# Optimization experiments

Hardware: AMD Instinct MI355X
Metric: run time of the kernel (lower is better)

Reference implementation:

```python
import jax, jax.numpy as jnp
import numpy as np

PAD = 1
STRIDE = (1, 1)
TEMPERATURE = 1.0


def setup_inputs() -> dict:
    key = jax.random.key(0)
    ks = jax.random.split(key, 5)
    x = jax.random.normal(ks[0], (16, 256, 56, 56), dtype=jnp.float32)
    kernels = jax.random.normal(ks[1], (8, 256, 256, 3, 3), dtype=jnp.float32)
    w1 = jax.random.normal(ks[2], (256, 64), dtype=jnp.float32) * 0.0625
    b1 = jnp.zeros((64,), dtype=jnp.float32)
    w2 = jax.random.normal(ks[3], (64, 8), dtype=jnp.float32) * 0.125
    b2 = jnp.zeros((8,), dtype=jnp.float32)
    return {"x": x, "kernels": kernels, "w1": w1, "b1": b1, "w2": w2, "b2": b2}


def _forward(x, kernels, w1, b1, w2, b2):
    # Attention: global average pool -> MLP -> softmax over kernels
    pooled = jnp.mean(x, axis=(2, 3))                      # [B, C]
    h = jax.nn.relu(pooled @ w1 + b1)                      # [B, H]
    scores = h @ w2 + b2                                   # [B, K]
    alphas = jax.nn.softmax(scores / TEMPERATURE, axis=-1) # [B, K]

    # Per-sample mixed kernels: [B, O, I, kh, kw]
    weighted = jnp.einsum('bk,koihw->boihw', alphas, kernels)

    # Per-sample conv2d (groups=1), vectorized over batch
    def conv_one(xi, wi):
        return jax.lax.conv_general_dilated(
            xi[None], wi, STRIDE, [(PAD, PAD), (PAD, PAD)],
            dimension_numbers=('NCHW', 'OIHW', 'NCHW'))[0]

    return jax.vmap(conv_one)(x, weighted)                 # [B, O, H, W]


def reference(x, kernels, w1, b1, w2, b2):
    return _forward(x, kernels, w1, b1, w2, b2)
```

## Files before the change

kernel.cpp:

```cpp
#include <hip/hip_runtime.h>
#include <hip/hip_bf16.h>
#include <stdint.h>

typedef __attribute__((ext_vector_type(8))) short bf16x8;
typedef __attribute__((ext_vector_type(4))) float f32x4;

#define BATCH 16
#define CH    256
#define HW    56
#define HWHW  3136
#define NK    8

#define XPT_BYTES   30408704ul
#define WK_BYTES    18874368ul
#define POOL_BYTES  16384ul
#define ALPHA_BYTES 512ul

__device__ __forceinline__ void gl_lds16(const void* g, void* l) {
    __builtin_amdgcn_global_load_lds((const __attribute__((address_space(1))) uint32_t*)g,
                                     (__attribute__((address_space(3))) uint32_t*)l, 16, 0, 0);
}

__device__ __forceinline__ float bf16bits_to_f32(short h) {
    return __uint_as_float(((uint32_t)(uint16_t)h) << 16);
}

__global__ void __launch_bounds__(256, 2)
xpose_pool_kernel(const float* __restrict__ x, __hip_bfloat16* __restrict__ xp,
                  float* __restrict__ pooled) {
    __shared__ short tile[2 * 56 * 256];
    const int tid = threadIdx.x;
    const int ys  = blockIdx.x;
    const int b   = blockIdx.y;
    const int y0  = ys * 2;

    const float* xb = x + (size_t)b * CH * HWHW + (size_t)y0 * HW;
    for (int it = 0; it < 28; ++it) {
        int idx = it * 256 + tid;
        int ch  = idx / 28;
        int xi  = idx - ch * 28;
        int r   = xi / 14;
        int x4  = (xi - r * 14) * 4;
        const float4 v = *(const float4*)(xb + (size_t)ch * HWHW + r * HW + x4);
        const float* vf = (const float*)&v;
#pragma unroll
        for (int j = 0; j < 4; ++j) {
            __hip_bfloat16 h = __float2bfloat16(vf[j]);
            tile[(r * 56 + x4 + j) * 256 + (ch ^ (((x4 & 7) | j) << 3))] = *(const short*)&h;
        }
    }
    __syncthreads();

    {
        float s = 0.f;
        const int ch = tid;
        for (int r = 0; r < 2; ++r)
            for (int xx = 0; xx < 56; ++xx)
                s += bf16bits_to_f32(tile[(r * 56 + xx) * 256 + (ch ^ ((xx & 7) << 3))]);
        atomicAdd(&pooled[b * 256 + ch], s * (1.0f / 3136.0f));
    }

    __hip_bfloat16* dst0 = xp + ((size_t)(b * 58 + y0 + 1) * 64 + 1) * 256;
    for (int it = 0; it < 14; ++it) {
        int idx = it * 256 + tid;
        int ch0 = (idx & 31) * 8;
        int pos = idx >> 5;
        int r = pos / 56, xx = pos - (pos / 56) * 56;
        bf16x8 vv = *(const bf16x8*)&tile[(r * 56 + xx) * 256 + (ch0 ^ ((xx & 7) << 3))];
        *(bf16x8*)(dst0 + ((size_t)(r * 64 + xx)) * 256 + ch0) = vv;
    }

    bf16x8 z = {};
    if (tid < 128) {
        int r   = tid >> 6;
        int c2  = (tid >> 5) & 1;
        int ch0 = (tid & 31) * 8;
        *(bf16x8*)(xp + ((size_t)(b * 58 + y0 + 1 + r) * 64 + (c2 ? 57 : 0)) * 256 + ch0) = z;
    }
    if (ys == 0 || ys == 27) {
        int p = (ys == 0) ? 0 : 57;
        __hip_bfloat16* rowp = xp + (size_t)(b * 58 + p) * 64 * 256;
        for (int it = tid; it < 2048; it += 256)
            *(bf16x8*)(rowp + (size_t)it * 8) = z;
    }
}

__global__ void mlp_kernel(const float* __restrict__ pooled,
                           const float* __restrict__ w1, const float* __restrict__ b1,
                           const float* __restrict__ w2, const float* __restrict__ b2,
                           float* __restrict__ alphas) {
    __shared__ float hs[16][64];
    __shared__ float sc[16][8];
    int t = threadIdx.x;
    for (int idx = t; idx < 16 * 64; idx += 256) {
        int b = idx >> 6, j = idx & 63;
        float acc = b1[j];
        const float* pb = pooled + b * 256;
        for (int c = 0; c < 256; ++c) acc += pb[c] * w1[c * 64 + j];
        hs[b][j] = fmaxf(acc, 0.0f);
    }
    __syncthreads();
    if (t < 128) {
        int b = t >> 3, k = t & 7;
        float acc = b2[k];
        for (int j = 0; j < 64; ++j) acc += hs[b][j] * w2[j * 8 + k];
        sc[b][k] = acc;
    }
    __syncthreads();
    if (t < 16) {
        float m = -1e30f;
        for (int k = 0; k < 8; ++k) m = fmaxf(m, sc[t][k]);
        float s = 0.f, e[8];
        for (int k = 0; k < 8; ++k) { e[k] = expf(sc[t][k] - m); s += e[k]; }
        float inv = 1.0f / s;
        for (int k = 0; k < 8; ++k) alphas[t * 8 + k] = e[k] * inv;
    }
}

__global__ void wmix_kernel(const float* __restrict__ kern, const float* __restrict__ alphas,
                            __hip_bfloat16* __restrict__ wk) {
    __shared__ float al[16][8];
    int t = threadIdx.x;
    if (t < 128) al[t >> 3][t & 7] = alphas[t];
    __syncthreads();
    int idx = blockIdx.x * 256 + t;
    float kv[8][9];
    const float* kp = kern + (size_t)idx * 9;
#pragma unroll
    for (int k = 0; k < 8; ++k)
#pragma unroll
        for (int q = 0; q < 9; ++q) kv[k][q] = kp[(size_t)k * 589824 + q];
#pragma unroll 1
    for (int b = 0; b < 16; ++b) {
#pragma unroll
        for (int q = 0; q < 9; ++q) {
            float acc = 0.f;
#pragma unroll
            for (int k = 0; k < 8; ++k) acc += al[b][k] * kv[k][q];
            wk[(((size_t)(b * 9 + q) * 256) << 8) + idx] = __float2bfloat16(acc);
        }
    }
}

__global__ void __launch_bounds__(256, 2)
conv_kernel(const __hip_bfloat16* __restrict__ xpT, const __hip_bfloat16* __restrict__ wk,
            float* __restrict__ out) {
    __shared__ short lds_x[2][6 * 64 * 32];
    __shared__ short lds_a[2][128 * 32];

    const int tid   = threadIdx.x;
    const int lane  = tid & 63;
    const int g     = lane >> 4;
    const int l15   = lane & 15;
    const int w     = tid >> 6;
    const int wm    = w >> 1;
    const int wn    = w & 1;
    const int w64   = tid & ~63;

    const int flat  = blockIdx.x;
    const int swzid = (flat & 7) * 56 + (flat >> 3);
    const int b     = swzid / 28;
    const int rem   = swzid - b * 28;
    const int mtile = rem & 1;
    const int y0    = (rem >> 1) * 4;

    int cellb[7], c3[7], rr[7], cc[7];
#pragma unroll
    for (int fn = 0; fn < 7; ++fn) {
        int n = wn * 112 + fn * 16 + l15;
        int r = n / 56, c = n % 56;
        rr[fn] = r; cc[fn] = c;
        cellb[fn] = r * 64 + c;
        c3[fn] = c & 3;
    }
    const int aoff = (wm * 64 + l15) * 64 + ((g ^ (l15 & 3)) << 4);

    f32x4 acc[4][7];
#pragma unroll
    for (int fm = 0; fm < 4; ++fm)
#pragma unroll
        for (int fn = 0; fn < 7; ++fn) acc[fm][fn] = (f32x4){0.f, 0.f, 0.f, 0.f};

    const size_t xb = ((size_t)b * 58 + y0) * 64 * 256;

#define STAGE_X(CI, BUF)                                                            \
    do {                                                                            \
        _Pragma("unroll")                                                           \
        for (int it = 0; it < 6; ++it) {                                            \
            int idx = it * 256 + tid;                                               \
            int slot = idx & 3, cell = idx >> 2;                                    \
            int c = cell & 63;                                                      \
            int tslot = slot ^ (c & 3);                                             \
            const __hip_bfloat16* src = xpT + xb + (size_t)cell * 256 + (CI) * 32 + tslot * 8; \
            gl_lds16(src, (char*)lds_x[BUF] + (it * 256 + w64) * 16);               \
        }                                                                           \
    } while (0)

#define STAGE_A(CI, KK, BUF)                                                        \
    do {                                                                            \
        const size_t wbase = ((size_t)((b * 9 + (KK)) * 256 + mtile * 128)) << 8;   \
        _Pragma("unroll")                                                           \
        for (int it = 0; it < 2; ++it) {                                            \
            int idx = it * 256 + tid;                                               \
            int slot = idx & 3, o = idx >> 2;                                       \
            int tslot = slot ^ (o & 3);                                             \
            const __hip_bfloat16* src = wk + wbase + ((size_t)o << 8) + (CI) * 32 + tslot * 8; \
            gl_lds16(src, (char*)lds_a[BUF] + (it * 256 + w64) * 16);               \
        }                                                                           \
    } while (0)

    STAGE_X(0, 0);
    STAGE_A(0, 0, 0);
    __syncthreads();

    int cab = 0, cxb = 0;
    int kk = 0, kh = 0, kw = 0, ci = 0;
#pragma unroll 1
    for (int s = 0; s < 72; ++s) {
        int nkk = kk + 1, nci = ci;
        if (nkk == 9) { nkk = 0; ++nci; }
        if (s < 71) {
            STAGE_A(nci, nkk, cab ^ 1);
            if (kk == 8) STAGE_X(nci, cxb ^ 1);
        }

        bf16x8 af[4];
#pragma unroll
        for (int fm = 0; fm < 4; ++fm)
            af[fm] = *(const bf16x8*)((const char*)lds_a[cab] + aoff + fm * 1024);
#pragma unroll
        for (int fn = 0; fn < 7; ++fn) {
            int cell = cellb[fn] + kh * 64 + kw;
            int slot = g ^ ((c3[fn] + kw) & 3);
            bf16x8 bfv = *(const bf16x8*)((const char*)lds_x[cxb] + cell * 64 + (slot << 4));
#pragma unroll
            for (int fm = 0; fm < 4; ++fm)
                acc[fm][fn] = __builtin_amdgcn_mfma_f32_16x16x32_bf16(af[fm], bfv, acc[fm][fn], 0, 0, 0);
        }

        __syncthreads();
        cab ^= 1;
        if (kk == 8) cxb ^= 1;
        kk = nkk; ci = nci;
        if (++kw == 3) { kw = 0; if (++kh == 3) kh = 0; }
    }

    const int mbase = mtile * 128 + wm * 64;
#pragma unroll
    for (int fm = 0; fm < 4; ++fm)
#pragma unroll
        for (int fn = 0; fn < 7; ++fn) {
            int o = mbase + fm * 16 + 4 * g;
            float* op = out + (((size_t)b * 256 + o) * 56 + (y0 + rr[fn])) * 56 + cc[fn];
#pragma unroll
            for (int r = 0; r < 4; ++r) op[(size_t)r * HWHW] = acc[fm][fn][r];
        }
#undef STAGE_X
#undef STAGE_A
}

extern "C" void kernel_launch(void* const* d_in, const int* in_sizes, int n_in,
                              void* d_out, int out_size, void* d_ws, size_t ws_size,
                              hipStream_t stream) {
    const float* x    = (const float*)d_in[0];
    const float* kern = (const float*)d_in[1];
    const float* w1   = (const float*)d_in[2];
    const float* b1   = (const float*)d_in[3];
    const float* w2   = (const float*)d_in[4];
    const float* b2   = (const float*)d_in[5];
    float* out = (float*)d_out;

    char* wsp = (char*)d_ws;
    __hip_bfloat16* xpT    = (__hip_bfloat16*)wsp;
    __hip_bfloat16* wkbuf  = (__hip_bfloat16*)(wsp + XPT_BYTES);
    float*          pooled = (float*)(wsp + XPT_BYTES + WK_BYTES);
    float*          alphas = (float*)(wsp + XPT_BYTES + WK_BYTES + POOL_BYTES);

    hipMemsetAsync(pooled, 0, POOL_BYTES, stream);

    xpose_pool_kernel<<<dim3(28, 16), dim3(256), 0, stream>>>(x, xpT, pooled);
    mlp_kernel<<<dim3(1), dim3(256), 0, stream>>>(pooled, w1, b1, w2, b2, alphas);
    wmix_kernel<<<dim3(256), dim3(256), 0, stream>>>(kern, alphas, wkbuf);
    conv_kernel<<<dim3(448), dim3(256), 0, stream>>>(xpT, wkbuf, out);
}
```

Measured before the change: 251.0 us.

## Load conv weights directly from global in MFMA fragment layout, drop LDS weight staging

The weight-mixing kernel now writes mixed bf16 weights in a pre-swizzled layout matching the MFMA A-fragment order, so the conv kernel reads A fragments straight from global/L2 instead of staging them through LDS. This removes one LDS buffer and the per-tap barrier, leaving one sync per input-channel chunk with all nine taps unrolled. The X staging swizzle changes to a (c>>1)-based XOR, and the MLP is split across 16 blocks with a parallel first-layer reduction. The trade-off is that every wave fetches its A fragments from global memory with no reuse through LDS, which raises L2 traffic and exposes load latency in the MFMA loop.

```diff
diff --git a/kernel.cpp b/kernel.cpp
--- a/kernel.cpp
+++ b/kernel.cpp
@@ -85,35 +85,45 @@
     }
 }
 
-__global__ void mlp_kernel(const float* __restrict__ pooled,
-                           const float* __restrict__ w1, const float* __restrict__ b1,
-                           const float* __restrict__ w2, const float* __restrict__ b2,
-                           float* __restrict__ alphas) {
-    __shared__ float hs[16][64];
-    __shared__ float sc[16][8];
+__global__ void __launch_bounds__(256)
+mlp_kernel(const float* __restrict__ pooled,
+           const float* __restrict__ w1, const float* __restrict__ b1,
+           const float* __restrict__ w2, const float* __restrict__ b2,
+           float* __restrict__ alphas) {
+    const int b = blockIdx.x;
+    __shared__ float pl[256];
+    __shared__ float hp[4][64];
+    __shared__ float h[64];
+    __shared__ float sc[8];
     int t = threadIdx.x;
-    for (int idx = t; idx < 16 * 64; idx += 256) {
-        int b = idx >> 6, j = idx & 63;
-        float acc = b1[j];
-        const float* pb = pooled + b * 256;
-        for (int c = 0; c < 256; ++c) acc += pb[c] * w1[c * 64 + j];
-        hs[b][j] = fmaxf(acc, 0.0f);
-    }
-    __syncthreads();
-    if (t < 128) {
-        int b = t >> 3, k = t & 7;
-        float acc = b2[k];
-        for (int j = 0; j < 64; ++j) acc += hs[b][j] * w2[j * 8 + k];
-        sc[b][k] = acc;
-    }
-    __syncthreads();
-    if (t < 16) {
-        float m = -1e30f;
-        for (int k = 0; k < 8; ++k) m = fmaxf(m, sc[t][k]);
-        float s = 0.f, e[8];
-        for (int k = 0; k < 8; ++k) { e[k] = expf(sc[t][k] - m); s += e[k]; }
-        float inv = 1.0f / s;
-        for (int k = 0; k < 8; ++k) alphas[t * 8 + k] = e[k] * inv;
+    pl[t] = pooled[b * 256 + t];
+    __syncthreads();
+    int j = t & 63, part = t >> 6;
+    float s = 0.f;
+    const float* w1p = w1 + part * 64 * 64 + j;
+#pragma unroll 8
+    for (int c = 0; c < 64; ++c) s += pl[part * 64 + c] * w1p[c * 64];
+    hp[part][j] = s;
+    __syncthreads();
+    if (t < 64) h[t] = fmaxf(hp[0][t] + hp[1][t] + hp[2][t] + hp[3][t] + b1[t], 0.f);
+    __syncthreads();
+    if (t < 8) {
+        float acc = b2[t];
+#pragma unroll 8
+        for (int jj = 0; jj < 64; ++jj) acc += h[jj] * w2[jj * 8 + t];
+        sc[t] = acc;
+    }
+    __syncthreads();
+    if (t == 0) {
+        float m = sc[0];
+#pragma unroll
+        for (int k = 1; k < 8; ++k) m = fmaxf(m, sc[k]);
+        float ssum = 0.f, e[8];
+#pragma unroll
+        for (int k = 0; k < 8; ++k) { e[k] = expf(sc[k] - m); ssum += e[k]; }
+        float inv = 1.0f / ssum;
+#pragma unroll
+        for (int k = 0; k < 8; ++k) alphas[b * 8 + k] = e[k] * inv;
     }
 }
 
@@ -123,13 +133,17 @@
     int t = threadIdx.x;
     if (t < 128) al[t >> 3][t & 7] = alphas[t];
     __syncthreads();
-    int idx = blockIdx.x * 256 + t;
+    const int o = blockIdx.x, i = t;
+    const int idx = o * 256 + i;
+    const size_t ibase = (size_t)((i >> 5) * 16384 + ((o >> 4)) * 1024 + (o & 15) * 64 +
+                                  ((i >> 3) & 3) * 16 + (i & 7) * 2);
     float kv[8][9];
     const float* kp = kern + (size_t)idx * 9;
 #pragma unroll
     for (int k = 0; k < 8; ++k)
 #pragma unroll
         for (int q = 0; q < 9; ++q) kv[k][q] = kp[(size_t)k * 589824 + q];
+    char* wkb = (char*)wk;
 #pragma unroll 1
     for (int b = 0; b < 16; ++b) {
 #pragma unroll
@@ -137,7 +151,8 @@
             float acc = 0.f;
 #pragma unroll
             for (int k = 0; k < 8; ++k) acc += al[b][k] * kv[k][q];
-            wk[(((size_t)(b * 9 + q) * 256) << 8) + idx] = __float2bfloat16(acc);
+            __hip_bfloat16 h = __float2bfloat16(acc);
+            *(short*)(wkb + (size_t)(b * 9 + q) * 131072 + ibase) = *(const short*)&h;
         }
     }
 }
@@ -146,7 +161,6 @@
 conv_kernel(const __hip_bfloat16* __restrict__ xpT, const __hip_bfloat16* __restrict__ wk,
             float* __restrict__ out) {
     __shared__ short lds_x[2][6 * 64 * 32];
-    __shared__ short lds_a[2][128 * 32];
 
     const int tid   = threadIdx.x;
     const int lane  = tid & 63;
@@ -164,16 +178,14 @@
     const int mtile = rem & 1;
     const int y0    = (rem >> 1) * 4;
 
-    int cellb[7], c3[7], rr[7], cc[7];
+    int cellb[7], cc[7], rr[7];
 #pragma unroll
     for (int fn = 0; fn < 7; ++fn) {
         int n = wn * 112 + fn * 16 + l15;
         int r = n / 56, c = n % 56;
         rr[fn] = r; cc[fn] = c;
         cellb[fn] = r * 64 + c;
-        c3[fn] = c & 3;
-    }
-    const int aoff = (wm * 64 + l15) * 64 + ((g ^ (l15 & 3)) << 4);
+    }
 
     f32x4 acc[4][7];
 #pragma unroll
@@ -182,67 +194,51 @@
         for (int fn = 0; fn < 7; ++fn) acc[fm][fn] = (f32x4){0.f, 0.f, 0.f, 0.f};
 
     const size_t xb = ((size_t)b * 58 + y0) * 64 * 256;
+    const char* wkb = (const char*)wk + (size_t)(b * 9) * 131072 +
+                      (size_t)((mtile * 8 + wm * 4) * 1024 + l15 * 64 + g * 16);
 
 #define STAGE_X(CI, BUF)                                                            \
     do {                                                                            \
         _Pragma("unroll")                                                           \
         for (int it = 0; it < 6; ++it) {                                            \
             int idx = it * 256 + tid;                                               \
-            int slot = idx & 3, cell = idx >> 2;                                    \
+            int sg  = idx & 3, cell = idx >> 2;                                     \
             int c = cell & 63;                                                      \
-            int tslot = slot ^ (c & 3);                                             \
-            const __hip_bfloat16* src = xpT + xb + (size_t)cell * 256 + (CI) * 32 + tslot * 8; \
+            int h = sg ^ ((c >> 1) & 3);                                            \
+            const __hip_bfloat16* src = xpT + xb + (size_t)cell * 256 + (CI) * 32 + h * 8; \
             gl_lds16(src, (char*)lds_x[BUF] + (it * 256 + w64) * 16);               \
         }                                                                           \
     } while (0)
 
-#define STAGE_A(CI, KK, BUF)                                                        \
+#define STEP(KK)                                                                    \
     do {                                                                            \
-        const size_t wbase = ((size_t)((b * 9 + (KK)) * 256 + mtile * 128)) << 8;   \
+        bf16x8 af[4];                                                               \
         _Pragma("unroll")                                                           \
-        for (int it = 0; it < 2; ++it) {                                            \
-            int idx = it * 256 + tid;                                               \
-            int slot = idx & 3, o = idx >> 2;                                       \
-            int tslot = slot ^ (o & 3);                                             \
-            const __hip_bfloat16* src = wk + wbase + ((size_t)o << 8) + (CI) * 32 + tslot * 8; \
-            gl_lds16(src, (char*)lds_a[BUF] + (it * 256 + w64) * 16);               \
+        for (int fm = 0; fm < 4; ++fm)                                              \
+            af[fm] = *(const bf16x8*)(wkb + (size_t)((KK) * 131072 + ci * 16384 + fm * 1024)); \
+        const int kh = (KK) / 3, kw = (KK) % 3;                                     \
+        _Pragma("unroll")                                                           \
+        for (int fn = 0; fn < 7; ++fn) {                                            \
+            int cell = cellb[fn] + kh * 64 + kw;                                    \
+            int slot = g ^ (((cc[fn] + kw) >> 1) & 3);                              \
+            bf16x8 bfv = *(const bf16x8*)(xlds + cell * 64 + (slot << 4));          \
+            _Pragma("unroll")                                                       \
+            for (int fm = 0; fm < 4; ++fm)                                          \
+                acc[fm][fn] = __builtin_amdgcn_mfma_f32_16x16x32_bf16(af[fm], bfv, acc[fm][fn], 0, 0, 0); \
         }                                                                           \
     } while (0)
 
     STAGE_X(0, 0);
-    STAGE_A(0, 0, 0);
-    __syncthreads();
-
-    int cab = 0, cxb = 0;
-    int kk = 0, kh = 0, kw = 0, ci = 0;
+    __syncthreads();
+
 #pragma unroll 1
-    for (int s = 0; s < 72; ++s) {
-        int nkk = kk + 1, nci = ci;
-        if (nkk == 9) { nkk = 0; ++nci; }
-        if (s < 71) {
-            STAGE_A(nci, nkk, cab ^ 1);
-            if (kk == 8) STAGE_X(nci, cxb ^ 1);
-        }
-
-        bf16x8 af[4];
-#pragma unroll
-        for (int fm = 0; fm < 4; ++fm)
-            af[fm] = *(const bf16x8*)((const char*)lds_a[cab] + aoff + fm * 1024);
-#pragma unroll
-        for (int fn = 0; fn < 7; ++fn) {
-            int cell = cellb[fn] + kh * 64 + kw;
-            int slot = g ^ ((c3[fn] + kw) & 3);
-            bf16x8 bfv = *(const bf16x8*)((const char*)lds_x[cxb] + cell * 64 + (slot << 4));
-#pragma unroll
-            for (int fm = 0; fm < 4; ++fm)
-                acc[fm][fn] = __builtin_amdgcn_mfma_f32_16x16x32_bf16(af[fm], bfv, acc[fm][fn], 0, 0, 0);
-        }
-
-        __syncthreads();
-        cab ^= 1;
-        if (kk == 8) cxb ^= 1;
-        kk = nkk; ci = nci;
-        if (++kw == 3) { kw = 0; if (++kh == 3) kh = 0; }
+    for (int ci = 0; ci < 8; ++ci) {
+        const char* xlds = (const char*)lds_x[ci & 1];
+        if (ci < 7) STAGE_X(ci + 1, (ci & 1) ^ 1);
+        STEP(0); STEP(1); STEP(2);
+        STEP(3); STEP(4); STEP(5);
+        STEP(6); STEP(7); STEP(8);
+        if (ci < 7) __syncthreads();
     }
 
     const int mbase = mtile * 128 + wm * 64;
@@ -256,7 +252,7 @@
             for (int r = 0; r < 4; ++r) op[(size_t)r * HWHW] = acc[fm][fn][r];
         }
 #undef STAGE_X
-#undef STAGE_A
+#undef STEP
 }
 
 extern "C" void kernel_launch(void* const* d_in, const int* in_sizes, int n_in,
@@ -279,7 +275,7 @@
     hipMemsetAsync(pooled, 0, POOL_BYTES, stream);
 
     xpose_pool_kernel<<<dim3(28, 16), dim3(256), 0, stream>>>(x, xpT, pooled);
-    mlp_kernel<<<dim3(1), dim3(256), 0, stream>>>(pooled, w1, b1, w2, b2, alphas);
+    mlp_kernel<<<dim3(16), dim3(256), 0, stream>>>(pooled, w1, b1, w2, b2, alphas);
     wmix_kernel<<<dim3(256), dim3(256), 0, stream>>>(kern, alphas, wkbuf);
     conv_kernel<<<dim3(448), dim3(256), 0, stream>>>(xpT, wkbuf, out);
 }
```

New measurement: 244.1 us. 1.03x faster.
